# Performance work log

Hardware: AMD Instinct MI355X
Metric: run time of the kernel (lower is better)

The kernel has to match this reference:

```python
import jax, jax.numpy as jnp
import numpy as np

N, D = 8192, 1024
TEMPERATURE = 0.5
EPS = 1e-12  # matches torch F.normalize eps


def setup_inputs() -> dict:
    key = jax.random.key(0)
    k1, k2 = jax.random.split(key)
    view1 = jax.random.normal(k1, (N, D), dtype=jnp.float32)
    view2 = jax.random.normal(k2, (N, D), dtype=jnp.float32)
    return {"view1": view1, "view2": view2}


def _l2_normalize(x):
    # F.normalize(x, dim=1): x / max(||x||_2, eps)
    norm = jnp.sqrt(jnp.sum(x * x, axis=1, keepdims=True))
    return x / jnp.maximum(norm, EPS)


def reference(view1, view2):
    z1 = _l2_normalize(view1)
    z2 = _l2_normalize(view2)
    sim = jnp.einsum('nd,md->nm', z1, z2) / TEMPERATURE  # [N, N]
    # cross_entropy with labels = arange(N): mean over rows of -log_softmax[i, i]
    logprobs = jax.nn.log_softmax(sim, axis=1)
    diag = jnp.diagonal(logprobs)
    return -jnp.mean(diag)
```

## Files before the change

kernel.cpp:

```cpp
#include <hip/hip_runtime.h>
#include <hip/hip_bf16.h>

#define NROW 8192
#define DDIM 1024
#define TINV 2.0f
#define SCALE1 0x7F7F7F7F

typedef __attribute__((ext_vector_type(4))) float f32x4;
typedef __attribute__((ext_vector_type(4))) int   i32x4;
typedef __attribute__((ext_vector_type(8))) int   i32x8;

__device__ __forceinline__ void gload_lds16(const void* g, void* l) {
  __builtin_amdgcn_global_load_lds(
      (const __attribute__((address_space(1))) void*)g,
      (__attribute__((address_space(3))) void*)l, 16, 0, 0);
}

#define SBAR()  __builtin_amdgcn_s_barrier()
#define PRIO(x) __builtin_amdgcn_s_setprio(x)
#define VMCNT(N) asm volatile("s_waitcnt vmcnt(" #N ")" ::: "memory")

__device__ __forceinline__ unsigned f2fp8(float x) {
  unsigned b = __float_as_uint(x);
  unsigned sgn = (b >> 24) & 0x80u;
  float af = __uint_as_float(b & 0x7FFFFFFFu);
  if (af >= 448.0f) return sgn | 0x7Eu;
  if (af < 0.015625f) {
    unsigned q = (unsigned)__float2int_rn(af * 512.0f);
    return sgn | q;
  }
  unsigned ab = b & 0x7FFFFFFFu;
  unsigned m  = ab & 0x7FFFFFu;
  unsigned m3 = m >> 20;
  unsigned rem = m & 0xFFFFFu;
  unsigned rnd = (rem > 0x80000u) || (rem == 0x80000u && (m3 & 1u));
  unsigned e  = (ab >> 23) - 120u;
  return sgn | ((e << 3) + m3 + rnd);
}

__global__ __launch_bounds__(256) void normalize_diag(
    const float* __restrict__ v1, const float* __restrict__ v2,
    unsigned* __restrict__ z1, unsigned* __restrict__ z2,
    float* __restrict__ diag)
{
  const int row = blockIdx.x;
  const int t = threadIdx.x;
  const float4 a = ((const float4*)(v1 + (size_t)row * 1024))[t];
  const float4 b = ((const float4*)(v2 + (size_t)row * 1024))[t];
  float s1 = a.x*a.x + a.y*a.y + a.z*a.z + a.w*a.w;
  float s2 = b.x*b.x + b.y*b.y + b.z*b.z + b.w*b.w;
  float sd = a.x*b.x + a.y*b.y + a.z*b.z + a.w*b.w;
  #pragma unroll
  for (int m = 1; m < 64; m <<= 1) {
    s1 += __shfl_xor(s1, m);
    s2 += __shfl_xor(s2, m);
    sd += __shfl_xor(sd, m);
  }
  __shared__ float red[3][4];
  const int w = t >> 6;
  if ((t & 63) == 0) { red[0][w] = s1; red[1][w] = s2; red[2][w] = sd; }
  __syncthreads();
  s1 = red[0][0] + red[0][1] + red[0][2] + red[0][3];
  s2 = red[1][0] + red[1][1] + red[1][2] + red[1][3];
  sd = red[2][0] + red[2][1] + red[2][2] + red[2][3];
  const float i1 = 1.0f / fmaxf(sqrtf(s1), 1e-12f);
  const float i2 = 1.0f / fmaxf(sqrtf(s2), 1e-12f);
  if (t == 0) diag[row] = sd * i1 * i2 * TINV;
  const float sc1 = i1 * TINV;
  unsigned o1 = f2fp8(a.x*sc1) | (f2fp8(a.y*sc1) << 8)
              | (f2fp8(a.z*sc1) << 16) | (f2fp8(a.w*sc1) << 24);
  unsigned o2 = f2fp8(b.x*i2)  | (f2fp8(b.y*i2)  << 8)
              | (f2fp8(b.z*i2) << 16) | (f2fp8(b.w*i2)  << 24);
  z1[(size_t)row * 256 + t] = o1;
  z2[(size_t)row * 256 + t] = o2;
}

#define BM 128
#define BN 128
#define BK 128
#define KTILES (DDIM / BK)

__global__ __launch_bounds__(256, 2) void gemm_rowsum(
    const unsigned char* __restrict__ z1b,
    const unsigned char* __restrict__ z2b,
    float* __restrict__ partial)
{
  __shared__ __align__(16) unsigned char As[2][BM * BK];
  __shared__ __align__(16) unsigned char Bs[2][BN * BK];

  const int bid = blockIdx.x;
  const int bi = bid >> 6;
  const int bj = bid & 63;
  const int brow = bi * BM;
  const int bcol = bj * BN;
  const int t = threadIdx.x;
  const int w = t >> 6;
  const int lane = t & 63;
  const int wr = w >> 1;
  const int wc = w & 1;
  const int lcol = lane & 15;
  const int lgrp = lane >> 4;
  const int l7 = lcol & 7;
  const int sr = lane >> 3;
  const int sc = lane & 7;
  const int ssw = (sc ^ sr) << 4;

  f32x4 acc[4][4];
  #pragma unroll
  for (int i = 0; i < 4; ++i)
    #pragma unroll
    for (int j = 0; j < 4; ++j)
      acc[i][j] = (f32x4){0.f, 0.f, 0.f, 0.f};

#define STAGE_A(S, BUF, K0)                                                   \
  gload_lds16(z1b + (size_t)(brow + w*32 + (S)*8 + sr) * DDIM + (K0) + ssw,   \
              &As[BUF][(w*4 + (S)) * 1024])
#define STAGE_B(S, BUF, K0)                                                   \
  gload_lds16(z2b + (size_t)(bcol + w*32 + (S)*8 + sr) * DDIM + (K0) + ssw,   \
              &Bs[BUF][(w*4 + (S)) * 1024])

#define RDFRAG(DST, ARR, ROWB)                                                \
  do {                                                                        \
    const int rb_ = (ROWB);                                                   \
    i32x4 lo_ = *(const i32x4*)&ARR[rb_*128 + ((lgrp)     ^ l7)*16];          \
    i32x4 hi_ = *(const i32x4*)&ARR[rb_*128 + ((4 + lgrp) ^ l7)*16];          \
    DST[0]=lo_[0]; DST[1]=lo_[1]; DST[2]=lo_[2]; DST[3]=lo_[3];               \
    DST[4]=hi_[0]; DST[5]=hi_[1]; DST[6]=hi_[2]; DST[7]=hi_[3];               \
  } while (0)

#define RA(MT, BUF, DST) RDFRAG(DST, As[BUF], wr*64 + (MT)*16 + lcol)
#define RB(NT, BUF, DST) RDFRAG(DST, Bs[BUF], wc*64 + (NT)*16 + lcol)

#define MF(MT, NT, AA, BB)                                                    \
  acc[MT][NT] = __builtin_amdgcn_mfma_scale_f32_16x16x128_f8f6f4(             \
      AA, BB, acc[MT][NT], 0, 0, 0, SCALE1, 0, SCALE1)

  #pragma unroll
  for (int s = 0; s < 4; ++s) { STAGE_A(s, 0, 0); STAGE_B(s, 0, 0); }
  #pragma unroll
  for (int s = 0; s < 4; ++s) { STAGE_A(s, 1, BK); STAGE_B(s, 1, BK); }
  VMCNT(8);
  SBAR();

  i32x8 am0, am1, bn0, bn1, bn2, bn3;

  #pragma unroll 2
  for (int kt = 0; kt < KTILES; ++kt) {
    const int cur = kt & 1;
    const int k2 = (kt + 2) * BK;
    const bool pf2 = (kt + 2 < KTILES);

    RA(0, cur, am0); RA(1, cur, am1);
    RB(0, cur, bn0); RB(1, cur, bn1);
    SBAR();
    PRIO(1); MF(0,0,am0,bn0); MF(1,1,am1,bn1);
             MF(0,1,am0,bn1); MF(1,0,am1,bn0); PRIO(0);
    SBAR();

    RB(2, cur, bn2); RB(3, cur, bn3);
    SBAR();
    PRIO(1); MF(0,2,am0,bn2); MF(1,3,am1,bn3);
             MF(0,3,am0,bn3); MF(1,2,am1,bn2); PRIO(0);
    SBAR();

    RA(2, cur, am0); RA(3, cur, am1);
    if (pf2) { STAGE_B(0, cur, k2); STAGE_B(1, cur, k2);
               STAGE_B(2, cur, k2); STAGE_B(3, cur, k2); }
    SBAR();
    PRIO(1); MF(2,2,am0,bn2); MF(3,3,am1,bn3);
             MF(2,3,am0,bn3); MF(3,2,am1,bn2); PRIO(0);
    SBAR();

    if (pf2) { STAGE_A(0, cur, k2); STAGE_A(1, cur, k2);
               STAGE_A(2, cur, k2); STAGE_A(3, cur, k2); }
    PRIO(1); MF(2,0,am0,bn0); MF(3,1,am1,bn1);
             MF(2,1,am0,bn1); MF(3,0,am1,bn0); PRIO(0);
    if (pf2)                   VMCNT(8);
    else if (kt + 1 < KTILES)  VMCNT(0);
    SBAR();
  }

  float* rs = (float*)&As[0][0];
  #pragma unroll
  for (int mt = 0; mt < 4; ++mt) {
    #pragma unroll
    for (int r = 0; r < 4; ++r) {
      float s = __expf(acc[mt][0][r]) + __expf(acc[mt][1][r])
              + __expf(acc[mt][2][r]) + __expf(acc[mt][3][r]);
      s += __shfl_xor(s, 1);
      s += __shfl_xor(s, 2);
      s += __shfl_xor(s, 4);
      s += __shfl_xor(s, 8);
      if (lcol == 0) rs[wc * 128 + wr * 64 + mt * 16 + lgrp * 4 + r] = s;
    }
  }
  __syncthreads();
  if (t < 128)
    partial[(size_t)bj * NROW + brow + t] = rs[t] + rs[128 + t];
}

__global__ __launch_bounds__(256) void rowloss(
    const float* __restrict__ partial, const float* __restrict__ diag,
    float* __restrict__ blocksum)
{
  const int i = blockIdx.x * 256 + threadIdx.x;
  float s = 0.f;
  #pragma unroll 8
  for (int b = 0; b < 64; ++b) s += partial[(size_t)b * NROW + i];
  float loss = logf(s) - diag[i];
  #pragma unroll
  for (int m = 1; m < 64; m <<= 1) loss += __shfl_xor(loss, m);
  __shared__ float red[4];
  if ((threadIdx.x & 63) == 0) red[threadIdx.x >> 6] = loss;
  __syncthreads();
  if (threadIdx.x == 0)
    blocksum[blockIdx.x] = red[0] + red[1] + red[2] + red[3];
}

__global__ void finalize(const float* __restrict__ blocksum,
                         float* __restrict__ out)
{
  float s = (threadIdx.x < 32) ? blocksum[threadIdx.x] : 0.f;
  #pragma unroll
  for (int m = 1; m < 64; m <<= 1) s += __shfl_xor(s, m);
  if (threadIdx.x == 0) out[0] = s * (1.0f / NROW);
}

extern "C" void kernel_launch(void* const* d_in, const int* in_sizes, int n_in,
                              void* d_out, int out_size, void* d_ws, size_t ws_size,
                              hipStream_t stream) {
  const float* v1 = (const float*)d_in[0];
  const float* v2 = (const float*)d_in[1];
  float* out = (float*)d_out;

  char* ws = (char*)d_ws;
  unsigned char* z1 = (unsigned char*)ws;
  unsigned char* z2 = (unsigned char*)(ws + (size_t)NROW * DDIM);
  float* diag = (float*)(ws + (size_t)NROW * DDIM * 2);
  float* partial = (float*)(ws + (size_t)NROW * DDIM * 2 + (size_t)NROW * 4);
  float* blocksum = (float*)(ws + (size_t)NROW * DDIM * 2 + (size_t)NROW * 4
                             + (size_t)64 * NROW * 4);

  normalize_diag<<<NROW, 256, 0, stream>>>(v1, v2, (unsigned*)z1, (unsigned*)z2,
                                           diag);
  gemm_rowsum<<<(NROW / BM) * (NROW / BN), 256, 0, stream>>>(z1, z2, partial);
  rowloss<<<NROW / 256, 256, 0, stream>>>(partial, diag, blocksum);
  finalize<<<1, 64, 0, stream>>>(blocksum, out);
}
```

Measured before the change: 116.7 us.

## Enlarge GEMM block tile to 256x256 with 8 waves per block

Doubles the GEMM block tile from 128x128 to 256x256 and the block from 4 to 8 waves. Each wave now computes a 128x64 sub-tile with 8x4 MFMA accumulators, and the staging, fragment reads, row-sum reduction and partial-sum layout are reworked to match, with 32 column blocks instead of 64. The goal is more operand reuse per LDS byte and less global traffic for the FP8 operands. In exchange, LDS use per block grows to 128KB and register pressure roughly doubles, which may limit occupancy below the 2-blocks-per-CU launch bound. The grid also shrinks to 1024 blocks.

```diff
diff --git a/kernel.cpp b/kernel.cpp
--- a/kernel.cpp
+++ b/kernel.cpp
@@ -75,12 +75,12 @@
   z2[(size_t)row * 256 + t] = o2;
 }
 
-#define BM 128
-#define BN 128
+#define BM 256
+#define BN 256
 #define BK 128
 #define KTILES (DDIM / BK)
 
-__global__ __launch_bounds__(256, 2) void gemm_rowsum(
+__global__ __launch_bounds__(512, 2) void gemm_rowsum(
     const unsigned char* __restrict__ z1b,
     const unsigned char* __restrict__ z2b,
     float* __restrict__ partial)
@@ -89,15 +89,15 @@
   __shared__ __align__(16) unsigned char Bs[2][BN * BK];
 
   const int bid = blockIdx.x;
-  const int bi = bid >> 6;
-  const int bj = bid & 63;
+  const int bi = bid >> 5;
+  const int bj = bid & 31;
   const int brow = bi * BM;
   const int bcol = bj * BN;
   const int t = threadIdx.x;
   const int w = t >> 6;
   const int lane = t & 63;
-  const int wr = w >> 1;
-  const int wc = w & 1;
+  const int wr = w >> 2;
+  const int wc = w & 3;
   const int lcol = lane & 15;
   const int lgrp = lane >> 4;
   const int l7 = lcol & 7;
@@ -105,18 +105,18 @@
   const int sc = lane & 7;
   const int ssw = (sc ^ sr) << 4;
 
-  f32x4 acc[4][4];
-  #pragma unroll
-  for (int i = 0; i < 4; ++i)
+  f32x4 acc[8][4];
+  #pragma unroll
+  for (int i = 0; i < 8; ++i)
     #pragma unroll
     for (int j = 0; j < 4; ++j)
       acc[i][j] = (f32x4){0.f, 0.f, 0.f, 0.f};
 
 #define STAGE_A(S, BUF, K0)                                                   \
-  gload_lds16(z1b + (size_t)(brow + w*32 + (S)*8 + sr) * DDIM + (K0) + ssw,   \
+  gload_lds16(z1b + (size_t)(brow + (w*4 + (S))*8 + sr) * DDIM + (K0) + ssw,  \
               &As[BUF][(w*4 + (S)) * 1024])
 #define STAGE_B(S, BUF, K0)                                                   \
-  gload_lds16(z2b + (size_t)(bcol + w*32 + (S)*8 + sr) * DDIM + (K0) + ssw,   \
+  gload_lds16(z2b + (size_t)(bcol + (w*4 + (S))*8 + sr) * DDIM + (K0) + ssw,  \
               &Bs[BUF][(w*4 + (S)) * 1024])
 
 #define RDFRAG(DST, ARR, ROWB)                                                \
@@ -128,8 +128,8 @@
     DST[4]=hi_[0]; DST[5]=hi_[1]; DST[6]=hi_[2]; DST[7]=hi_[3];               \
   } while (0)
 
-#define RA(MT, BUF, DST) RDFRAG(DST, As[BUF], wr*64 + (MT)*16 + lcol)
-#define RB(NT, BUF, DST) RDFRAG(DST, Bs[BUF], wc*64 + (NT)*16 + lcol)
+#define RA(MT, BUF, DST) RDFRAG(DST, As[BUF], wr*128 + (MT)*16 + lcol)
+#define RB(NT, BUF, DST) RDFRAG(DST, Bs[BUF], wc*64  + (NT)*16 + lcol)
 
 #define MF(MT, NT, AA, BB)                                                    \
   acc[MT][NT] = __builtin_amdgcn_mfma_scale_f32_16x16x128_f8f6f4(             \
@@ -142,7 +142,7 @@
   VMCNT(8);
   SBAR();
 
-  i32x8 am0, am1, bn0, bn1, bn2, bn3;
+  i32x8 am[4], bn0, bn1, bn2, bn3;
 
   #pragma unroll 2
   for (int kt = 0; kt < KTILES; ++kt) {
@@ -150,31 +150,41 @@
     const int k2 = (kt + 2) * BK;
     const bool pf2 = (kt + 2 < KTILES);
 
-    RA(0, cur, am0); RA(1, cur, am1);
+    #pragma unroll
+    for (int mi = 0; mi < 4; ++mi) RA(mi, cur, am[mi]);
     RB(0, cur, bn0); RB(1, cur, bn1);
     SBAR();
-    PRIO(1); MF(0,0,am0,bn0); MF(1,1,am1,bn1);
-             MF(0,1,am0,bn1); MF(1,0,am1,bn0); PRIO(0);
+    PRIO(1);
+    MF(0,0,am[0],bn0); MF(1,1,am[1],bn1); MF(2,0,am[2],bn0); MF(3,1,am[3],bn1);
+    MF(0,1,am[0],bn1); MF(1,0,am[1],bn0); MF(2,1,am[2],bn1); MF(3,0,am[3],bn0);
+    PRIO(0);
     SBAR();
 
     RB(2, cur, bn2); RB(3, cur, bn3);
     SBAR();
-    PRIO(1); MF(0,2,am0,bn2); MF(1,3,am1,bn3);
-             MF(0,3,am0,bn3); MF(1,2,am1,bn2); PRIO(0);
-    SBAR();
-
-    RA(2, cur, am0); RA(3, cur, am1);
+    PRIO(1);
+    MF(0,2,am[0],bn2); MF(1,3,am[1],bn3); MF(2,2,am[2],bn2); MF(3,3,am[3],bn3);
+    MF(0,3,am[0],bn3); MF(1,2,am[1],bn2); MF(2,3,am[2],bn3); MF(3,2,am[3],bn2);
+    PRIO(0);
+    SBAR();
+
+    #pragma unroll
+    for (int mi = 0; mi < 4; ++mi) RA(mi + 4, cur, am[mi]);
     if (pf2) { STAGE_B(0, cur, k2); STAGE_B(1, cur, k2);
                STAGE_B(2, cur, k2); STAGE_B(3, cur, k2); }
     SBAR();
-    PRIO(1); MF(2,2,am0,bn2); MF(3,3,am1,bn3);
-             MF(2,3,am0,bn3); MF(3,2,am1,bn2); PRIO(0);
+    PRIO(1);
+    MF(4,2,am[0],bn2); MF(5,3,am[1],bn3); MF(6,2,am[2],bn2); MF(7,3,am[3],bn3);
+    MF(4,3,am[0],bn3); MF(5,2,am[1],bn2); MF(6,3,am[2],bn3); MF(7,2,am[3],bn2);
+    PRIO(0);
     SBAR();
 
     if (pf2) { STAGE_A(0, cur, k2); STAGE_A(1, cur, k2);
                STAGE_A(2, cur, k2); STAGE_A(3, cur, k2); }
-    PRIO(1); MF(2,0,am0,bn0); MF(3,1,am1,bn1);
-             MF(2,1,am0,bn1); MF(3,0,am1,bn0); PRIO(0);
+    PRIO(1);
+    MF(4,0,am[0],bn0); MF(5,1,am[1],bn1); MF(6,0,am[2],bn0); MF(7,1,am[3],bn1);
+    MF(4,1,am[0],bn1); MF(5,0,am[1],bn0); MF(6,1,am[2],bn1); MF(7,0,am[3],bn0);
+    PRIO(0);
     if (pf2)                   VMCNT(8);
     else if (kt + 1 < KTILES)  VMCNT(0);
     SBAR();
@@ -182,7 +192,7 @@
 
   float* rs = (float*)&As[0][0];
   #pragma unroll
-  for (int mt = 0; mt < 4; ++mt) {
+  for (int mt = 0; mt < 8; ++mt) {
     #pragma unroll
     for (int r = 0; r < 4; ++r) {
       float s = __expf(acc[mt][0][r]) + __expf(acc[mt][1][r])
@@ -191,12 +201,14 @@
       s += __shfl_xor(s, 2);
       s += __shfl_xor(s, 4);
       s += __shfl_xor(s, 8);
-      if (lcol == 0) rs[wc * 128 + wr * 64 + mt * 16 + lgrp * 4 + r] = s;
+      if (lcol == 0)
+        rs[wc * 256 + wr * 128 + mt * 16 + lgrp * 4 + r] = s;
     }
   }
   __syncthreads();
-  if (t < 128)
-    partial[(size_t)bj * NROW + brow + t] = rs[t] + rs[128 + t];
+  if (t < 256)
+    partial[(size_t)bj * NROW + brow + t] =
+        rs[t] + rs[256 + t] + rs[512 + t] + rs[768 + t];
 }
 
 __global__ __launch_bounds__(256) void rowloss(
@@ -206,7 +218,7 @@
   const int i = blockIdx.x * 256 + threadIdx.x;
   float s = 0.f;
   #pragma unroll 8
-  for (int b = 0; b < 64; ++b) s += partial[(size_t)b * NROW + i];
+  for (int b = 0; b < 32; ++b) s += partial[(size_t)b * NROW + i];
   float loss = logf(s) - diag[i];
   #pragma unroll
   for (int m = 1; m < 64; m <<= 1) loss += __shfl_xor(loss, m);
@@ -239,11 +251,11 @@
   float* diag = (float*)(ws + (size_t)NROW * DDIM * 2);
   float* partial = (float*)(ws + (size_t)NROW * DDIM * 2 + (size_t)NROW * 4);
   float* blocksum = (float*)(ws + (size_t)NROW * DDIM * 2 + (size_t)NROW * 4
-                             + (size_t)64 * NROW * 4);
+                             + (size_t)32 * NROW * 4);
 
   normalize_diag<<<NROW, 256, 0, stream>>>(v1, v2, (unsigned*)z1, (unsigned*)z2,
                                            diag);
-  gemm_rowsum<<<(NROW / BM) * (NROW / BN), 256, 0, stream>>>(z1, z2, partial);
+  gemm_rowsum<<<(NROW / BM) * (NROW / BN), 512, 0, stream>>>(z1, z2, partial);
   rowloss<<<NROW / 256, 256, 0, stream>>>(partial, diag, blocksum);
   finalize<<<1, 64, 0, stream>>>(blocksum, out);
 }
```

Measured after the change: 397.7 us. 241% more time.

## Enlarge GEMM block tile to 256x128 with 8 waves and restructure MFMA schedule

Applied to the files above, without the earlier changes.

Doubles the block's M tile to 256 rows, runs 512 threads per block, and rewrites the global-to-LDS staging so each wave loads four A chunks and two B chunks. All four A fragments are now held in registers at once, which cuts the K-step loop from four barrier phases to three. The aim is more reuse of each B tile and fewer synchronisation points per K step. In exchange, each block needs about 96KB of LDS, so only one block fits per CU, and more fragment registers are live at once.

```diff
diff --git a/kernel.cpp b/kernel.cpp
--- a/kernel.cpp
+++ b/kernel.cpp
@@ -75,12 +75,12 @@
   z2[(size_t)row * 256 + t] = o2;
 }
 
-#define BM 128
+#define BM 256
 #define BN 128
 #define BK 128
 #define KTILES (DDIM / BK)
 
-__global__ __launch_bounds__(256, 2) void gemm_rowsum(
+__global__ __launch_bounds__(512, 2) void gemm_rowsum(
     const unsigned char* __restrict__ z1b,
     const unsigned char* __restrict__ z2b,
     float* __restrict__ partial)
@@ -113,11 +113,11 @@
       acc[i][j] = (f32x4){0.f, 0.f, 0.f, 0.f};
 
 #define STAGE_A(S, BUF, K0)                                                   \
-  gload_lds16(z1b + (size_t)(brow + w*32 + (S)*8 + sr) * DDIM + (K0) + ssw,   \
+  gload_lds16(z1b + (size_t)(brow + (w*4 + (S))*8 + sr) * DDIM + (K0) + ssw,  \
               &As[BUF][(w*4 + (S)) * 1024])
 #define STAGE_B(S, BUF, K0)                                                   \
-  gload_lds16(z2b + (size_t)(bcol + w*32 + (S)*8 + sr) * DDIM + (K0) + ssw,   \
-              &Bs[BUF][(w*4 + (S)) * 1024])
+  gload_lds16(z2b + (size_t)(bcol + (w*2 + (S))*8 + sr) * DDIM + (K0) + ssw,  \
+              &Bs[BUF][(w*2 + (S)) * 1024])
 
 #define RDFRAG(DST, ARR, ROWB)                                                \
   do {                                                                        \
@@ -136,46 +136,44 @@
       AA, BB, acc[MT][NT], 0, 0, 0, SCALE1, 0, SCALE1)
 
   #pragma unroll
-  for (int s = 0; s < 4; ++s) { STAGE_A(s, 0, 0); STAGE_B(s, 0, 0); }
-  #pragma unroll
-  for (int s = 0; s < 4; ++s) { STAGE_A(s, 1, BK); STAGE_B(s, 1, BK); }
-  VMCNT(8);
+  for (int s = 0; s < 4; ++s) STAGE_A(s, 0, 0);
+  STAGE_B(0, 0, 0); STAGE_B(1, 0, 0);
+  #pragma unroll
+  for (int s = 0; s < 4; ++s) STAGE_A(s, 1, BK);
+  STAGE_B(0, 1, BK); STAGE_B(1, 1, BK);
+  VMCNT(6);
   SBAR();
 
-  i32x8 am0, am1, bn0, bn1, bn2, bn3;
-
-  #pragma unroll 2
+  i32x8 am0, am1, am2, am3, bn0, bn1, bn2, bn3;
+
   for (int kt = 0; kt < KTILES; ++kt) {
     const int cur = kt & 1;
     const int k2 = (kt + 2) * BK;
     const bool pf2 = (kt + 2 < KTILES);
 
-    RA(0, cur, am0); RA(1, cur, am1);
+    RA(0, cur, am0); RA(1, cur, am1); RA(2, cur, am2); RA(3, cur, am3);
     RB(0, cur, bn0); RB(1, cur, bn1);
     SBAR();
-    PRIO(1); MF(0,0,am0,bn0); MF(1,1,am1,bn1);
-             MF(0,1,am0,bn1); MF(1,0,am1,bn0); PRIO(0);
+    PRIO(1);
+    MF(0,0,am0,bn0); MF(1,1,am1,bn1); MF(2,0,am2,bn0); MF(3,1,am3,bn1);
+    MF(0,1,am0,bn1); MF(1,0,am1,bn0); MF(2,1,am2,bn1); MF(3,0,am3,bn0);
+    PRIO(0);
     SBAR();
 
     RB(2, cur, bn2); RB(3, cur, bn3);
-    SBAR();
-    PRIO(1); MF(0,2,am0,bn2); MF(1,3,am1,bn3);
-             MF(0,3,am0,bn3); MF(1,2,am1,bn2); PRIO(0);
-    SBAR();
-
-    RA(2, cur, am0); RA(3, cur, am1);
-    if (pf2) { STAGE_B(0, cur, k2); STAGE_B(1, cur, k2);
-               STAGE_B(2, cur, k2); STAGE_B(3, cur, k2); }
-    SBAR();
-    PRIO(1); MF(2,2,am0,bn2); MF(3,3,am1,bn3);
-             MF(2,3,am0,bn3); MF(3,2,am1,bn2); PRIO(0);
-    SBAR();
-
     if (pf2) { STAGE_A(0, cur, k2); STAGE_A(1, cur, k2);
                STAGE_A(2, cur, k2); STAGE_A(3, cur, k2); }
-    PRIO(1); MF(2,0,am0,bn0); MF(3,1,am1,bn1);
-             MF(2,1,am0,bn1); MF(3,0,am1,bn0); PRIO(0);
-    if (pf2)                   VMCNT(8);
+    SBAR();
+    PRIO(1);
+    MF(0,2,am0,bn2); MF(1,2,am1,bn2); MF(2,2,am2,bn2); MF(3,2,am3,bn2);
+    PRIO(0);
+    SBAR();
+
+    if (pf2) { STAGE_B(0, cur, k2); STAGE_B(1, cur, k2); }
+    PRIO(1);
+    MF(0,3,am0,bn3); MF(1,3,am1,bn3); MF(2,3,am2,bn3); MF(3,3,am3,bn3);
+    PRIO(0);
+    if (pf2)                   VMCNT(6);
     else if (kt + 1 < KTILES)  VMCNT(0);
     SBAR();
   }
@@ -191,12 +189,13 @@
       s += __shfl_xor(s, 2);
       s += __shfl_xor(s, 4);
       s += __shfl_xor(s, 8);
-      if (lcol == 0) rs[wc * 128 + wr * 64 + mt * 16 + lgrp * 4 + r] = s;
+      if (lcol == 0)
+        rs[wc * 256 + wr * 64 + mt * 16 + lgrp * 4 + r] = s;
     }
   }
   __syncthreads();
-  if (t < 128)
-    partial[(size_t)bj * NROW + brow + t] = rs[t] + rs[128 + t];
+  if (t < 256)
+    partial[(size_t)bj * NROW + brow + t] = rs[t] + rs[256 + t];
 }
 
 __global__ __launch_bounds__(256) void rowloss(
@@ -243,7 +242,7 @@
 
   normalize_diag<<<NROW, 256, 0, stream>>>(v1, v2, (unsigned*)z1, (unsigned*)z2,
                                            diag);
-  gemm_rowsum<<<(NROW / BM) * (NROW / BN), 256, 0, stream>>>(z1, z2, partial);
+  gemm_rowsum<<<(NROW / BM) * (NROW / BN), 512, 0, stream>>>(z1, z2, partial);
   rowloss<<<NROW / 256, 256, 0, stream>>>(partial, diag, blocksum);
   finalize<<<1, 64, 0, stream>>>(blocksum, out);
 }
```

Result: slower. 409.7 us (+250.9%).

## Write FP8 operands in MFMA fragment layout and load fragments directly from global

Applied to the files above, without the earlier changes.

The normalize kernel now writes the FP8 z1/z2 matrices in a tiled layout that matches the MFMA 16x16x128 operand fragments. The GEMM drops the LDS staging, swizzling and barriers and instead loads each fragment straight from global memory into registers, double-buffered across K tiles. This removes LDS traffic and barrier synchronisation. In exchange, operands shared between waves are no longer reused through LDS, so every wave fetches its own data from L2/global and global load latency is more exposed.

```diff
diff --git a/kernel.cpp b/kernel.cpp
--- a/kernel.cpp
+++ b/kernel.cpp
@@ -9,16 +9,6 @@
 typedef __attribute__((ext_vector_type(4))) float f32x4;
 typedef __attribute__((ext_vector_type(4))) int   i32x4;
 typedef __attribute__((ext_vector_type(8))) int   i32x8;
-
-__device__ __forceinline__ void gload_lds16(const void* g, void* l) {
-  __builtin_amdgcn_global_load_lds(
-      (const __attribute__((address_space(1))) void*)g,
-      (__attribute__((address_space(3))) void*)l, 16, 0, 0);
-}
-
-#define SBAR()  __builtin_amdgcn_s_barrier()
-#define PRIO(x) __builtin_amdgcn_s_setprio(x)
-#define VMCNT(N) asm volatile("s_waitcnt vmcnt(" #N ")" ::: "memory")
 
 __device__ __forceinline__ unsigned f2fp8(float x) {
   unsigned b = __float_as_uint(x);
@@ -38,9 +28,10 @@
   return sgn | ((e << 3) + m3 + rnd);
 }
 
+
 __global__ __launch_bounds__(256) void normalize_diag(
     const float* __restrict__ v1, const float* __restrict__ v2,
-    unsigned* __restrict__ z1, unsigned* __restrict__ z2,
+    unsigned char* __restrict__ z1f, unsigned char* __restrict__ z2f,
     float* __restrict__ diag)
 {
   const int row = blockIdx.x;
@@ -71,28 +62,24 @@
               | (f2fp8(a.z*sc1) << 16) | (f2fp8(a.w*sc1) << 24);
   unsigned o2 = f2fp8(b.x*i2)  | (f2fp8(b.y*i2)  << 8)
               | (f2fp8(b.z*i2) << 16) | (f2fp8(b.w*i2)  << 24);
-  z1[(size_t)row * 256 + t] = o1;
-  z2[(size_t)row * 256 + t] = o2;
-}
-
-#define BM 128
-#define BN 128
-#define BK 128
-#define KTILES (DDIM / BK)
+  const size_t off = (size_t)(row >> 4) * 16384 + (size_t)(t >> 2) * 256
+                   + (size_t)(row & 15) * 16 + (size_t)(t & 3) * 4;
+  *(unsigned*)(z1f + off) = o1;
+  *(unsigned*)(z2f + off) = o2;
+}
+
+#define KTILES 8
 
 __global__ __launch_bounds__(256, 2) void gemm_rowsum(
-    const unsigned char* __restrict__ z1b,
-    const unsigned char* __restrict__ z2b,
+    const unsigned char* __restrict__ z1f,
+    const unsigned char* __restrict__ z2f,
     float* __restrict__ partial)
 {
-  __shared__ __align__(16) unsigned char As[2][BM * BK];
-  __shared__ __align__(16) unsigned char Bs[2][BN * BK];
+  __shared__ float rs[2][128];
 
   const int bid = blockIdx.x;
   const int bi = bid >> 6;
   const int bj = bid & 63;
-  const int brow = bi * BM;
-  const int bcol = bj * BN;
   const int t = threadIdx.x;
   const int w = t >> 6;
   const int lane = t & 63;
@@ -100,10 +87,11 @@
   const int wc = w & 1;
   const int lcol = lane & 15;
   const int lgrp = lane >> 4;
-  const int l7 = lcol & 7;
-  const int sr = lane >> 3;
-  const int sc = lane & 7;
-  const int ssw = (sc ^ sr) << 4;
+
+  const unsigned char* Abase = z1f + (size_t)(bi*8 + wr*4) * 16384
+                             + (size_t)lgrp * 512 + (size_t)lcol * 16;
+  const unsigned char* Bbase = z2f + (size_t)(bj*8 + wc*4) * 16384
+                             + (size_t)lgrp * 512 + (size_t)lcol * 16;
 
   f32x4 acc[4][4];
   #pragma unroll
@@ -112,75 +100,42 @@
     for (int j = 0; j < 4; ++j)
       acc[i][j] = (f32x4){0.f, 0.f, 0.f, 0.f};
 
-#define STAGE_A(S, BUF, K0)                                                   \
-  gload_lds16(z1b + (size_t)(brow + w*32 + (S)*8 + sr) * DDIM + (K0) + ssw,   \
-              &As[BUF][(w*4 + (S)) * 1024])
-#define STAGE_B(S, BUF, K0)                                                   \
-  gload_lds16(z2b + (size_t)(bcol + w*32 + (S)*8 + sr) * DDIM + (K0) + ssw,   \
-              &Bs[BUF][(w*4 + (S)) * 1024])
-
-#define RDFRAG(DST, ARR, ROWB)                                                \
-  do {                                                                        \
-    const int rb_ = (ROWB);                                                   \
-    i32x4 lo_ = *(const i32x4*)&ARR[rb_*128 + ((lgrp)     ^ l7)*16];          \
-    i32x4 hi_ = *(const i32x4*)&ARR[rb_*128 + ((4 + lgrp) ^ l7)*16];          \
-    DST[0]=lo_[0]; DST[1]=lo_[1]; DST[2]=lo_[2]; DST[3]=lo_[3];               \
-    DST[4]=hi_[0]; DST[5]=hi_[1]; DST[6]=hi_[2]; DST[7]=hi_[3];               \
+#define LF(DST, BASE, MT, KT) do {                                            \
+    i32x4 lo_ = *(const i32x4*)((BASE) + (size_t)(MT)*16384 + (size_t)(KT)*2048); \
+    i32x4 hi_ = *(const i32x4*)((BASE) + (size_t)(MT)*16384 + (size_t)(KT)*2048 + 256); \
+    DST = __builtin_shufflevector(lo_, hi_, 0,1,2,3,4,5,6,7);                 \
   } while (0)
 
-#define RA(MT, BUF, DST) RDFRAG(DST, As[BUF], wr*64 + (MT)*16 + lcol)
-#define RB(NT, BUF, DST) RDFRAG(DST, Bs[BUF], wc*64 + (NT)*16 + lcol)
+#define LOADTILE(A0,A1,A2,A3,B0,B1,B2,B3,KT)                                  \
+  do { LF(A0, Abase, 0, KT); LF(A1, Abase, 1, KT);                            \
+       LF(A2, Abase, 2, KT); LF(A3, Abase, 3, KT);                            \
+       LF(B0, Bbase, 0, KT); LF(B1, Bbase, 1, KT);                            \
+       LF(B2, Bbase, 2, KT); LF(B3, Bbase, 3, KT); } while (0)
 
 #define MF(MT, NT, AA, BB)                                                    \
   acc[MT][NT] = __builtin_amdgcn_mfma_scale_f32_16x16x128_f8f6f4(             \
       AA, BB, acc[MT][NT], 0, 0, 0, SCALE1, 0, SCALE1)
 
-  #pragma unroll
-  for (int s = 0; s < 4; ++s) { STAGE_A(s, 0, 0); STAGE_B(s, 0, 0); }
-  #pragma unroll
-  for (int s = 0; s < 4; ++s) { STAGE_A(s, 1, BK); STAGE_B(s, 1, BK); }
-  VMCNT(8);
-  SBAR();
-
-  i32x8 am0, am1, bn0, bn1, bn2, bn3;
-
-  #pragma unroll 2
-  for (int kt = 0; kt < KTILES; ++kt) {
-    const int cur = kt & 1;
-    const int k2 = (kt + 2) * BK;
-    const bool pf2 = (kt + 2 < KTILES);
-
-    RA(0, cur, am0); RA(1, cur, am1);
-    RB(0, cur, bn0); RB(1, cur, bn1);
-    SBAR();
-    PRIO(1); MF(0,0,am0,bn0); MF(1,1,am1,bn1);
-             MF(0,1,am0,bn1); MF(1,0,am1,bn0); PRIO(0);
-    SBAR();
-
-    RB(2, cur, bn2); RB(3, cur, bn3);
-    SBAR();
-    PRIO(1); MF(0,2,am0,bn2); MF(1,3,am1,bn3);
-             MF(0,3,am0,bn3); MF(1,2,am1,bn2); PRIO(0);
-    SBAR();
-
-    RA(2, cur, am0); RA(3, cur, am1);
-    if (pf2) { STAGE_B(0, cur, k2); STAGE_B(1, cur, k2);
-               STAGE_B(2, cur, k2); STAGE_B(3, cur, k2); }
-    SBAR();
-    PRIO(1); MF(2,2,am0,bn2); MF(3,3,am1,bn3);
-             MF(2,3,am0,bn3); MF(3,2,am1,bn2); PRIO(0);
-    SBAR();
-
-    if (pf2) { STAGE_A(0, cur, k2); STAGE_A(1, cur, k2);
-               STAGE_A(2, cur, k2); STAGE_A(3, cur, k2); }
-    PRIO(1); MF(2,0,am0,bn0); MF(3,1,am1,bn1);
-             MF(2,1,am0,bn1); MF(3,0,am1,bn0); PRIO(0);
-    if (pf2)                   VMCNT(8);
-    else if (kt + 1 < KTILES)  VMCNT(0);
-    SBAR();
-  }
-
-  float* rs = (float*)&As[0][0];
+#define MFMA16(A0,A1,A2,A3,B0,B1,B2,B3)                                       \
+  do { MF(0,0,A0,B0); MF(1,1,A1,B1); MF(2,2,A2,B2); MF(3,3,A3,B3);            \
+       MF(0,1,A0,B1); MF(1,0,A1,B0); MF(2,3,A2,B3); MF(3,2,A3,B2);            \
+       MF(0,2,A0,B2); MF(1,3,A1,B3); MF(2,0,A2,B0); MF(3,1,A3,B1);            \
+       MF(0,3,A0,B3); MF(1,2,A1,B2); MF(2,1,A2,B1); MF(3,0,A3,B0); } while (0)
+
+  i32x8 pa0,pa1,pa2,pa3, pb0,pb1,pb2,pb3;
+  i32x8 qa0,qa1,qa2,qa3, qb0,qb1,qb2,qb3;
+
+  LOADTILE(pa0,pa1,pa2,pa3, pb0,pb1,pb2,pb3, 0);
+
+  #pragma unroll
+  for (int kt = 0; kt < KTILES; kt += 2) {
+    LOADTILE(qa0,qa1,qa2,qa3, qb0,qb1,qb2,qb3, kt + 1);
+    MFMA16(pa0,pa1,pa2,pa3, pb0,pb1,pb2,pb3);
+    if (kt + 2 < KTILES)
+      LOADTILE(pa0,pa1,pa2,pa3, pb0,pb1,pb2,pb3, kt + 2);
+    MFMA16(qa0,qa1,qa2,qa3, qb0,qb1,qb2,qb3);
+  }
+
   #pragma unroll
   for (int mt = 0; mt < 4; ++mt) {
     #pragma unroll
@@ -191,12 +146,13 @@
       s += __shfl_xor(s, 2);
       s += __shfl_xor(s, 4);
       s += __shfl_xor(s, 8);
-      if (lcol == 0) rs[wc * 128 + wr * 64 + mt * 16 + lgrp * 4 + r] = s;
+      if (lcol == 0)
+        rs[wc][wr * 64 + mt * 16 + lgrp * 4 + r] = s;
     }
   }
   __syncthreads();
   if (t < 128)
-    partial[(size_t)bj * NROW + brow + t] = rs[t] + rs[128 + t];
+    partial[(size_t)bj * NROW + bi * 128 + t] = rs[0][t] + rs[1][t];
 }
 
 __global__ __launch_bounds__(256) void rowloss(
@@ -234,16 +190,15 @@
   float* out = (float*)d_out;
 
   char* ws = (char*)d_ws;
-  unsigned char* z1 = (unsigned char*)ws;
-  unsigned char* z2 = (unsigned char*)(ws + (size_t)NROW * DDIM);
+  unsigned char* z1f = (unsigned char*)ws;
+  unsigned char* z2f = (unsigned char*)(ws + (size_t)NROW * DDIM);
   float* diag = (float*)(ws + (size_t)NROW * DDIM * 2);
   float* partial = (float*)(ws + (size_t)NROW * DDIM * 2 + (size_t)NROW * 4);
   float* blocksum = (float*)(ws + (size_t)NROW * DDIM * 2 + (size_t)NROW * 4
                              + (size_t)64 * NROW * 4);
 
-  normalize_diag<<<NROW, 256, 0, stream>>>(v1, v2, (unsigned*)z1, (unsigned*)z2,
-                                           diag);
-  gemm_rowsum<<<(NROW / BM) * (NROW / BN), 256, 0, stream>>>(z1, z2, partial);
+  normalize_diag<<<NROW, 256, 0, stream>>>(v1, v2, z1f, z2f, diag);
+  gemm_rowsum<<<64 * 64, 256, 0, stream>>>(z1f, z2f, partial);
   rowloss<<<NROW / 256, 256, 0, stream>>>(partial, diag, blocksum);
   finalize<<<1, 64, 0, stream>>>(blocksum, out);
 }
```

After: 456.4 us. 291% more time.
